# Kernel tuning notes

Hardware: AMD Instinct MI355X
Metric: run time of the kernel (lower is better)

The kernel has to match this reference:

```python
import jax, jax.numpy as jnp
import numpy as np

B, P, L, M, L_EVAL = 8, 16, 256, 16, 2048
T_MAX = 100.0


def setup_inputs() -> dict:
    key = jax.random.key(0)
    k1, k2, k3, k4, k5 = jax.random.split(key, 5)
    # sorted event times per path (Hawkes event streams are ordered)
    event_times = jnp.sort(jax.random.uniform(k1, (B, P, L), dtype=jnp.float32) * T_MAX, axis=-1)
    # parameters are assumed already positive (post-softplus) -> uniform [0,1)
    mu = jax.random.uniform(k2, (B, M, P, L), dtype=jnp.float32)
    alpha = jax.random.uniform(k3, (B, M, P, L), dtype=jnp.float32)
    beta = jax.random.uniform(k4, (B, M, P, L), dtype=jnp.float32)
    query_times = jax.random.uniform(k5, (B, P, L_EVAL), dtype=jnp.float32) * T_MAX
    return {"query_times": query_times, "event_times": event_times,
            "mu": mu, "alpha": alpha, "beta": beta}


def reference(query_times, event_times, mu, alpha, beta):
    # query_times: [B,P,Le]; event_times: [B,P,L]; mu/alpha/beta: [B,M,P,L]
    b, m, p, l = mu.shape
    le = query_times.shape[-1]
    # index of latest event strictly before each query time (mask + max, as original)
    past_mask = event_times[:, :, None, :] < query_times[:, :, :, None]  # [B,P,Le,L]
    idx = jnp.arange(l, dtype=jnp.int32)
    last_idx = jnp.max(jnp.where(past_mask, idx, -1), axis=-1)            # [B,P,Le]
    ci = jnp.clip(last_idx, 0, None)
    gi = jnp.broadcast_to(ci[:, None, :, :], (b, m, p, le))
    mu_last = jnp.take_along_axis(mu, gi, axis=3)
    alpha_last = jnp.take_along_axis(alpha, gi, axis=3)
    beta_last = jnp.take_along_axis(beta, gi, axis=3)
    t_last = jnp.take_along_axis(event_times, ci, axis=2)                 # [B,P,Le]
    t_last = jnp.where(last_idx == -1, jnp.zeros_like(t_last), t_last)
    delta_t = (query_times - t_last)[:, None, :, :]                       # [B,1,P,Le]
    base = mu_last + (alpha_last - mu_last) * jnp.exp(-beta_last * delta_t)
    return jax.nn.softplus(base)                                          # [B,M,P,Le]
```

## Files before the change

kernel.cpp:

```cpp
#include <hip/hip_runtime.h>
#include <float.h>

#define BB  8
#define PP  16
#define LL  256
#define MM  16
#define LE  2048
#define TILE 512
#define THREADS 256

__global__ __launch_bounds__(THREADS) void hawkes_intensity_kernel(
    const float* __restrict__ qt,
    const float* __restrict__ ev,
    const float* __restrict__ mu,
    const float* __restrict__ alpha,
    const float* __restrict__ beta,
    float* __restrict__ out)
{
    __shared__ float ev_s[LL + 1];
    __shared__ float mu_s[MM * LL];
    __shared__ float al_s[MM * LL];
    __shared__ float be_s[MM * LL];

    const int tiles_per_bp = LE / TILE;
    const int bp   = blockIdx.x / tiles_per_bp;
    const int tile = blockIdx.x % tiles_per_bp;
    const int b = bp / PP;
    const int p = bp % PP;
    const int t = threadIdx.x;

    ev_s[t] = ev[bp * LL + t];
    if (t == 0) ev_s[LL] = FLT_MAX;

    {
        const float4* mu4 = (const float4*)mu;
        const float4* al4 = (const float4*)alpha;
        const float4* be4 = (const float4*)beta;
        float4* mus4 = (float4*)mu_s;
        float4* als4 = (float4*)al_s;
        float4* bes4 = (float4*)be_s;
        #pragma unroll
        for (int i = t; i < MM * LL / 4; i += THREADS) {
            const int m  = i >> 6;
            const int l4 = i & 63;
            const int g  = ((b * MM + m) * PP + p) * (LL / 4) + l4;
            mus4[i] = mu4[g];
            als4[i] = al4[g];
            bes4[i] = be4[g];
        }
    }
    __syncthreads();

    const int le0 = tile * TILE;
    const float* qrow = qt + bp * LE + le0;

    #pragma unroll
    for (int k = 0; k < TILE; k += THREADS) {
        const int le = le0 + k + t;
        const float q = qrow[k + t];

        int lo = 0, hi = LL;
        #pragma unroll
        for (int s = 0; s < 9; ++s) {
            const int mid = (lo + hi) >> 1;
            if (ev_s[mid] < q) lo = mid + 1; else hi = mid;
        }
        const int cnt = lo;
        const int ci  = (cnt > 0) ? (cnt - 1) : 0;
        const float t_last = (cnt > 0) ? ev_s[ci] : 0.0f;
        const float dt = q - t_last;

        int o = ((b * MM) * PP + p) * LE + le;
        #pragma unroll
        for (int m = 0; m < MM; ++m) {
            const float mm = mu_s[m * LL + ci];
            const float aa = al_s[m * LL + ci];
            const float bb = be_s[m * LL + ci];
            const float e  = __expf(-bb * dt);
            const float base = mm + (aa - mm) * e;
            out[o] = __logf(1.0f + __expf(base));
            o += PP * LE;
        }
    }
}

extern "C" void kernel_launch(void* const* d_in, const int* in_sizes, int n_in,
                              void* d_out, int out_size, void* d_ws, size_t ws_size,
                              hipStream_t stream) {
    const float* qt    = (const float*)d_in[0];
    const float* ev    = (const float*)d_in[1];
    const float* mu    = (const float*)d_in[2];
    const float* alpha = (const float*)d_in[3];
    const float* beta  = (const float*)d_in[4];
    float* out = (float*)d_out;

    const int nblocks = (BB * PP) * (LE / TILE);
    hawkes_intensity_kernel<<<nblocks, THREADS, 0, stream>>>(qt, ev, mu, alpha, beta, out);
}
```

Before: 77.22 us.

## Split search and evaluation into two kernels with interleaved param LDS and float4 stores

Splits the work into two kernels. The first runs the binary search for each query and writes the last-event index and delta-t to workspace. The second kernel is split over groups of four marks: it stages mu/alpha/beta interleaved as float4 in shared memory, so each gather is a single LDS load, and writes four consecutive outputs per thread as float4 stores. This cuts the shared-memory footprint per block (raising occupancy) and vectorises the dominant output writes, at the cost of an extra launch and a round trip through global workspace.

```diff
diff --git a/kernel.cpp b/kernel.cpp
--- a/kernel.cpp
+++ b/kernel.cpp
@@ -6,59 +6,30 @@
 #define LL  256
 #define MM  16
 #define LE  2048
-#define TILE 512
+#define NQ  (BB * PP * LE)
+
 #define THREADS 256
 
-__global__ __launch_bounds__(THREADS) void hawkes_intensity_kernel(
+__global__ __launch_bounds__(THREADS) void k_search(
     const float* __restrict__ qt,
     const float* __restrict__ ev,
-    const float* __restrict__ mu,
-    const float* __restrict__ alpha,
-    const float* __restrict__ beta,
-    float* __restrict__ out)
+    int*   __restrict__ ci_out,
+    float* __restrict__ dt_out)
 {
     __shared__ float ev_s[LL + 1];
-    __shared__ float mu_s[MM * LL];
-    __shared__ float al_s[MM * LL];
-    __shared__ float be_s[MM * LL];
-
-    const int tiles_per_bp = LE / TILE;
-    const int bp   = blockIdx.x / tiles_per_bp;
-    const int tile = blockIdx.x % tiles_per_bp;
-    const int b = bp / PP;
-    const int p = bp % PP;
+    const int bp   = blockIdx.x >> 2;
+    const int tile = blockIdx.x & 3;
     const int t = threadIdx.x;
 
     ev_s[t] = ev[bp * LL + t];
     if (t == 0) ev_s[LL] = FLT_MAX;
-
-    {
-        const float4* mu4 = (const float4*)mu;
-        const float4* al4 = (const float4*)alpha;
-        const float4* be4 = (const float4*)beta;
-        float4* mus4 = (float4*)mu_s;
-        float4* als4 = (float4*)al_s;
-        float4* bes4 = (float4*)be_s;
-        #pragma unroll
-        for (int i = t; i < MM * LL / 4; i += THREADS) {
-            const int m  = i >> 6;
-            const int l4 = i & 63;
-            const int g  = ((b * MM + m) * PP + p) * (LL / 4) + l4;
-            mus4[i] = mu4[g];
-            als4[i] = al4[g];
-            bes4[i] = be4[g];
-        }
-    }
     __syncthreads();
 
-    const int le0 = tile * TILE;
-    const float* qrow = qt + bp * LE + le0;
-
+    const int base = bp * LE + tile * 512;
     #pragma unroll
-    for (int k = 0; k < TILE; k += THREADS) {
-        const int le = le0 + k + t;
-        const float q = qrow[k + t];
-
+    for (int k = 0; k < 512; k += THREADS) {
+        const int idx = base + k + t;
+        const float q = qt[idx];
         int lo = 0, hi = LL;
         #pragma unroll
         for (int s = 0; s < 9; ++s) {
@@ -68,19 +39,69 @@
         const int cnt = lo;
         const int ci  = (cnt > 0) ? (cnt - 1) : 0;
         const float t_last = (cnt > 0) ? ev_s[ci] : 0.0f;
-        const float dt = q - t_last;
+        ci_out[idx] = ci;
+        dt_out[idx] = q - t_last;
+    }
+}
 
-        int o = ((b * MM) * PP + p) * LE + le;
+#define MG   4
+#define QT2  1024
+
+__global__ __launch_bounds__(THREADS) void k_eval(
+    const float* __restrict__ mu,
+    const float* __restrict__ alpha,
+    const float* __restrict__ beta,
+    const int*   __restrict__ ci_in,
+    const float* __restrict__ dt_in,
+    float* __restrict__ out)
+{
+    __shared__ float4 pr[MG * LL];
+
+    const int mg   =  blockIdx.x & 3;
+    const int tile = (blockIdx.x >> 2) & 1;
+    const int bp   =  blockIdx.x >> 3;
+    const int b = bp / PP;
+    const int p = bp % PP;
+    const int t = threadIdx.x;
+
+    {
+        const float4* mu4 = (const float4*)mu;
+        const float4* al4 = (const float4*)alpha;
+        const float4* be4 = (const float4*)beta;
+        const int i  = t;
+        const int m  = i >> 6;
+        const int l4 = i & 63;
+        const int g  = ((b * MM + mg * MG + m) * PP + p) * (LL / 4) + l4;
+        const float4 mv = mu4[g];
+        const float4 av = al4[g];
+        const float4 bv = be4[g];
+        const int o = m * LL + l4 * 4;
+        pr[o + 0] = make_float4(mv.x, av.x, bv.x, 0.0f);
+        pr[o + 1] = make_float4(mv.y, av.y, bv.y, 0.0f);
+        pr[o + 2] = make_float4(mv.z, av.z, bv.z, 0.0f);
+        pr[o + 3] = make_float4(mv.w, av.w, bv.w, 0.0f);
+    }
+    __syncthreads();
+
+    const int q0  = tile * QT2 + 4 * t;
+    const int idx = bp * LE + q0;
+    const int4   ci4 = *(const int4*)  (ci_in + idx);
+    const float4 dt4 = *(const float4*)(dt_in + idx);
+    const int ci[4] = {ci4.x, ci4.y, ci4.z, ci4.w};
+    const float dt[4] = {dt4.x, dt4.y, dt4.z, dt4.w};
+
+    #pragma unroll
+    for (int m = 0; m < MG; ++m) {
+        float r[4];
         #pragma unroll
-        for (int m = 0; m < MM; ++m) {
-            const float mm = mu_s[m * LL + ci];
-            const float aa = al_s[m * LL + ci];
-            const float bb = be_s[m * LL + ci];
-            const float e  = __expf(-bb * dt);
-            const float base = mm + (aa - mm) * e;
-            out[o] = __logf(1.0f + __expf(base));
-            o += PP * LE;
+        for (int j = 0; j < 4; ++j) {
+            const float4 pm = pr[m * LL + ci[j]];
+            const float e = __expf(-pm.z * dt[j]);
+            const float v = pm.x + (pm.y - pm.x) * e;
+            r[j] = __logf(1.0f + __expf(v));
         }
+        float4* dst = (float4*)(out + ((size_t)(b * MM + mg * MG + m) * PP + p) * LE + q0);
+        *dst = make_float4(r[0], r[1], r[2], r[3]);
     }
 }
 
@@ -94,6 +115,10 @@
     const float* beta  = (const float*)d_in[4];
     float* out = (float*)d_out;
 
-    const int nblocks = (BB * PP) * (LE / TILE);
-    hawkes_intensity_kernel<<<nblocks, THREADS, 0, stream>>>(qt, ev, mu, alpha, beta, out);
+    int*   ci_ws = (int*)d_ws;
+    float* dt_ws = (float*)((char*)d_ws + (size_t)NQ * sizeof(int));
+
+    k_search<<<(BB * PP) * 4, THREADS, 0, stream>>>(qt, ev, ci_ws, dt_ws);
+    k_eval<<<(BB * PP) * (MM / MG) * (LE / QT2), THREADS, 0, stream>>>(
+        mu, alpha, beta, ci_ws, dt_ws, out);
 }
```

After: 79.29 us. 2.7% more time.
